# Kernel tuning notes

Hardware: AMD Instinct MI355X
Metric: run time of the kernel (lower is better)

The kernel has to match this reference:

```python
import jax, jax.numpy as jnp
import numpy as np
from jax import lax

INPUT_SIZE = 256
HIDDEN_SIZE = 512
NUM_LAYERS = 2
T = 2048
B = 64


def setup_inputs() -> dict:
    key = jax.random.key(0)
    k1, k2, k3, k4, k5 = jax.random.split(key, 5)
    fan_g = INPUT_SIZE + HIDDEN_SIZE
    inp = {
        "input": jax.random.normal(k1, (T, B, INPUT_SIZE), dtype=jnp.float32),
        "gate_w": jax.random.uniform(k2, (HIDDEN_SIZE, fan_g), dtype=jnp.float32,
                                     minval=-1.0, maxval=1.0) / np.sqrt(fan_g),
        "gate_b": jax.random.uniform(k3, (HIDDEN_SIZE,), dtype=jnp.float32,
                                     minval=-1.0, maxval=1.0) / np.sqrt(fan_g),
        "out_w": jax.random.uniform(k4, (INPUT_SIZE, HIDDEN_SIZE), dtype=jnp.float32,
                                    minval=-1.0, maxval=1.0) / np.sqrt(HIDDEN_SIZE),
        "out_b": jax.random.uniform(k5, (INPUT_SIZE,), dtype=jnp.float32,
                                    minval=-1.0, maxval=1.0) / np.sqrt(HIDDEN_SIZE),
        "name": 0,  # unused forward arg in the original module
    }
    return inp


def reference(input, gate_w, gate_b, out_w, out_b, name):
    # input: [T, B, input_size]
    batch = input.shape[1]
    h0 = jnp.zeros((batch, HIDDEN_SIZE), dtype=jnp.float32)
    c0 = jnp.zeros((batch, HIDDEN_SIZE), dtype=jnp.float32)

    def step(carry, x_t):
        h, c = carry
        combined = jnp.concatenate([h, x_t], axis=1)          # [B, H+I]
        g = combined @ gate_w.T + gate_b
        s = jax.nn.sigmoid(g)                                 # f = i = o = sigmoid(g)
        ch = jnp.tanh(g)                                      # cell_helper
        c = c * s + ch * s
        h = jnp.tanh(c) * s
        return (h, c), None

    carry = (h0, c0)
    # hidden/cell carry over across layers; every layer re-consumes the same input
    for _ in range(NUM_LAYERS):
        carry, _ = lax.scan(step, carry, input)
    h, _ = carry
    output = h @ out_w.T + out_b                              # [B, input_size]
    return output
```

## Files before the change

### kernel.cpp

```cpp
#include <hip/hip_runtime.h>
#include <stdint.h>

#define T_STEPS 2048
#define BATCH   64
#define IN_SZ   256
#define HID     512
#define FANG    768
#define NLAYER  2
#define TOT_STEPS (T_STEPS*NLAYER)

typedef _Float16 h2 __attribute__((ext_vector_type(2)));
typedef unsigned long long u64;
typedef unsigned int u32;

__device__ __forceinline__ float dot2f(h2 a, h2 b, float c) {
#if __has_builtin(__builtin_amdgcn_fdot2)
    return __builtin_amdgcn_fdot2(a, b, c, false);
#else
    return c + (float)a.x * (float)b.x + (float)a.y * (float)b.y;
#endif
}

__device__ __forceinline__ u32 packh2(float a, float b) {
    h2 t{(_Float16)a, (_Float16)b};
    return __builtin_bit_cast(u32, t);
}
__device__ __forceinline__ h2 bch2(float v) { return __builtin_bit_cast(h2, v); }
__device__ __forceinline__ h2 bch2u(u32 v)  { return __builtin_bit_cast(h2, v); }

__device__ __forceinline__ u64 ld_llc(const u64* p) {
    return __hip_atomic_load(p, __ATOMIC_RELAXED, __HIP_MEMORY_SCOPE_AGENT);
}
__device__ __forceinline__ void st_llc(u64* p, u64 v) {
    __hip_atomic_store(p, v, __ATOMIC_RELAXED, __HIP_MEMORY_SCOPE_AGENT);
}

template<int CTRL>
__device__ __forceinline__ float dpp_add(float x) {
    int xi = __builtin_bit_cast(int, x);
    int yi = __builtin_amdgcn_update_dpp(0, xi, CTRL, 0xf, 0xf, true);
    return x + __builtin_bit_cast(float, yi);
}
__device__ __forceinline__ float reduce16(float x) {
    x = dpp_add<0xB1>(x);
    x = dpp_add<0x4E>(x);
    x = dpp_add<0x124>(x);
    x = dpp_add<0x128>(x);
    return x;
}

__global__ __launch_bounds__(256) void xproj_kernel(
    const float* __restrict__ input,
    const float* __restrict__ gate_w,
    const float* __restrict__ gate_b,
    u32* __restrict__ xp16)
{
    __shared__ _Float16 Bs[64][264];
    __shared__ _Float16 As[64][264];

    const int jt = blockIdx.x;
    const int mg = blockIdx.y;
    const int tid = threadIdx.x;
    const int tx = tid & 15, ty = tid >> 4;
    const int j0 = jt * 64;

    #pragma unroll
    for (int l = 0; l < 16; ++l) {
        int e = tid + l * 256;
        int i = e >> 6, kq = e & 63;
        float4 v = *(const float4*)&gate_w[(size_t)(j0 + i) * FANG + HID + kq * 4];
        *(h2*)&Bs[i][kq * 4]     = h2{(_Float16)v.x, (_Float16)v.y};
        *(h2*)&Bs[i][kq * 4 + 2] = h2{(_Float16)v.z, (_Float16)v.w};
    }

    const float4 gb = *(const float4*)&gate_b[j0 + tx * 4];

    for (int mt = 0; mt < 32; ++mt) {
        const int m0 = (mg * 32 + mt) * 64;
        __syncthreads();
        #pragma unroll
        for (int l = 0; l < 16; ++l) {
            int e = tid + l * 256;
            int i = e >> 6, kq = e & 63;
            float4 v = *(const float4*)&input[(size_t)(m0 + i) * IN_SZ + kq * 4];
            *(h2*)&As[i][kq * 4]     = h2{(_Float16)v.x, (_Float16)v.y};
            *(h2*)&As[i][kq * 4 + 2] = h2{(_Float16)v.z, (_Float16)v.w};
        }
        __syncthreads();

        float acc[4][4] = {};
        #pragma unroll
        for (int q = 0; q < 32; ++q) {
            const int k = ((q + tx) & 31) * 8;
            float4 av[4], bv[4];
            #pragma unroll
            for (int i = 0; i < 4; ++i)  av[i] = *(const float4*)&As[ty * 4 + i][k];
            #pragma unroll
            for (int jj = 0; jj < 4; ++jj) bv[jj] = *(const float4*)&Bs[tx * 4 + jj][k];
            #pragma unroll
            for (int i = 0; i < 4; ++i) {
                h2 a0 = bch2(av[i].x), a1 = bch2(av[i].y);
                h2 a2 = bch2(av[i].z), a3 = bch2(av[i].w);
                #pragma unroll
                for (int jj = 0; jj < 4; ++jj) {
                    acc[i][jj] = dot2f(a0, bch2(bv[jj].x), acc[i][jj]);
                    acc[i][jj] = dot2f(a1, bch2(bv[jj].y), acc[i][jj]);
                    acc[i][jj] = dot2f(a2, bch2(bv[jj].z), acc[i][jj]);
                    acc[i][jj] = dot2f(a3, bch2(bv[jj].w), acc[i][jj]);
                }
            }
        }

        #pragma unroll
        for (int i = 0; i < 4; ++i) {
            uint2 ww = { packh2(acc[i][0] + gb.x, acc[i][1] + gb.y),
                         packh2(acc[i][2] + gb.z, acc[i][3] + gb.w) };
            *(uint2*)&xp16[(size_t)(m0 + ty * 4 + i) * 256 + ((j0 + tx * 4) >> 1)] = ww;
        }
    }
}

__global__ __launch_bounds__(512, 2) void lstm_kernel(
    const float* __restrict__ gate_w,
    const u32* __restrict__ xp16,
    u64* __restrict__ hx)
{
    const int blk = blockIdx.x;
    const int s   = blk >> 6;
    const int b   = blk & 63;
    const int tid = threadIdx.x;
    const int g   = tid >> 4;
    const int c   = tid & 15;
    const int j0  = s * 128 + g * 4;

    __shared__ u32 hl[2][256];

    h2 w2[64];
    #pragma unroll
    for (int u = 0; u < 4; ++u) {
        const int kb = (((s + u) & 3) * 64 + c * 4) * 2;
        #pragma unroll
        for (int rr = 0; rr < 4; ++rr) {
            const float* wr = gate_w + (size_t)(j0 + rr) * FANG + kb;
            float4 v0 = *(const float4*)(wr);
            float4 v1 = *(const float4*)(wr + 4);
            w2[rr * 16 + u * 4 + 0] = h2{(_Float16)v0.x, (_Float16)v0.y};
            w2[rr * 16 + u * 4 + 1] = h2{(_Float16)v0.z, (_Float16)v0.w};
            w2[rr * 16 + u * 4 + 2] = h2{(_Float16)v1.x, (_Float16)v1.y};
            w2[rr * 16 + u * 4 + 3] = h2{(_Float16)v1.z, (_Float16)v1.w};
        }
    }

    const int si  = tid >> 6;
    const int qs  = si + (si >= s);
    const int prw = qs * 64 + (tid & 63);

    if (tid < 256) hl[0][tid] = 0;

    float cval = 0.0f;

    for (int st = 0; st < TOT_STEPS; ++st) {
        const int t   = st & (T_STEPS - 1);
        const int buf = st & 1;

        u32 xw = 0;
        if (c < 4) xw = xp16[((size_t)t * BATCH + b) * 256 + s * 64 + g * 2 + (c >> 1)];

        const u64* pp = hx + ((size_t)buf * BATCH + b) * 256 + prw;
        u64 pv = 0;
        if (tid < 192) pv = ld_llc(pp);

        __syncthreads();

        float a0 = 0.f, a1 = 0.f, a2 = 0.f, a3 = 0.f;
        {
            float4 rv = *(const float4*)&hl[buf][s * 64 + c * 4];
            h2 x0 = bch2(rv.x), x1 = bch2(rv.y), x2 = bch2(rv.z), x3 = bch2(rv.w);
            a0 = dot2f(w2[ 0], x0, a0); a0 = dot2f(w2[ 1], x1, a0);
            a0 = dot2f(w2[ 2], x2, a0); a0 = dot2f(w2[ 3], x3, a0);
            a1 = dot2f(w2[16], x0, a1); a1 = dot2f(w2[17], x1, a1);
            a1 = dot2f(w2[18], x2, a1); a1 = dot2f(w2[19], x3, a1);
            a2 = dot2f(w2[32], x0, a2); a2 = dot2f(w2[33], x1, a2);
            a2 = dot2f(w2[34], x2, a2); a2 = dot2f(w2[35], x3, a2);
            a3 = dot2f(w2[48], x0, a3); a3 = dot2f(w2[49], x1, a3);
            a3 = dot2f(w2[50], x2, a3); a3 = dot2f(w2[51], x3, a3);
        }

        if (tid < 192) {
            u64 v = pv;
            int spin = 0;
            while ((u32)(v >> 32) != (u32)st) {
                v = ld_llc(pp);
                if (++spin > (1 << 16)) break;
                if (spin > 64) __builtin_amdgcn_s_sleep(1);
            }
            hl[buf][prw] = (u32)v;
        }
        __syncthreads();

        #pragma unroll
        for (int u = 1; u < 4; ++u) {
            float4 rv = *(const float4*)&hl[buf][((s + u) & 3) * 64 + c * 4];
            h2 x0 = bch2(rv.x), x1 = bch2(rv.y), x2 = bch2(rv.z), x3 = bch2(rv.w);
            a0 = dot2f(w2[     u*4+0], x0, a0); a0 = dot2f(w2[     u*4+1], x1, a0);
            a0 = dot2f(w2[     u*4+2], x2, a0); a0 = dot2f(w2[     u*4+3], x3, a0);
            a1 = dot2f(w2[16 + u*4+0], x0, a1); a1 = dot2f(w2[16 + u*4+1], x1, a1);
            a1 = dot2f(w2[16 + u*4+2], x2, a1); a1 = dot2f(w2[16 + u*4+3], x3, a1);
            a2 = dot2f(w2[32 + u*4+0], x0, a2); a2 = dot2f(w2[32 + u*4+1], x1, a2);
            a2 = dot2f(w2[32 + u*4+2], x2, a2); a2 = dot2f(w2[32 + u*4+3], x3, a2);
            a3 = dot2f(w2[48 + u*4+0], x0, a3); a3 = dot2f(w2[48 + u*4+1], x1, a3);
            a3 = dot2f(w2[48 + u*4+2], x2, a3); a3 = dot2f(w2[48 + u*4+3], x3, a3);
        }

        a0 = reduce16(a0);
        a1 = reduce16(a1);
        a2 = reduce16(a2);
        a3 = reduce16(a3);

        float hf = 0.0f;
        if (c < 4) {
            float p = (c == 0) ? a0 : (c == 1) ? a1 : (c == 2) ? a2 : a3;
            h2 xp = bch2u(xw);
            float gg = p + (float)((c & 1) ? xp.y : xp.x);
            gg = fminf(fmaxf(gg, -30.0f), 30.0f);
            float sg = 1.0f / (1.0f + __expf(-gg));
            float e2 = __expf(2.0f * gg);
            float ch = (e2 - 1.0f) / (e2 + 1.0f);
            cval = cval * sg + ch * sg;
            float ca = fminf(fmaxf(cval, -15.0f), 15.0f);
            float e3 = __expf(2.0f * ca);
            hf = ((e3 - 1.0f) / (e3 + 1.0f)) * sg;
        }
        float hfo = __shfl_down(hf, 1);
        if (c == 0 || c == 2) {
            const int w = s * 64 + g * 2 + (c >> 1);
            u32 pk = packh2(hf, hfo);
            st_llc(hx + ((size_t)((st + 1) & 1) * BATCH + b) * 256 + w,
                   (u64)pk | ((u64)(u32)(st + 1) << 32));
            hl[buf ^ 1][w] = pk;
        }
    }
}

__global__ __launch_bounds__(256) void out_kernel(
    const u64* __restrict__ hx,
    const float* __restrict__ out_w,
    const float* __restrict__ out_b,
    float* __restrict__ out)
{
    const int b  = blockIdx.x;
    const int jt = threadIdx.x;
    __shared__ float hrow[512];

    {
        u64 v = hx[(size_t)b * 256 + jt];
        h2 pr = bch2u((u32)v);
        hrow[2 * jt]     = (float)pr.x;
        hrow[2 * jt + 1] = (float)pr.y;
    }
    __syncthreads();

    float acc = out_b[jt];
    const float* wr = out_w + (size_t)jt * HID;
    #pragma unroll 8
    for (int k = 0; k < HID; ++k)
        acc += hrow[k] * wr[k];
    out[(size_t)b * IN_SZ + jt] = acc;
}

extern "C" void kernel_launch(void* const* d_in, const int* in_sizes, int n_in,
                              void* d_out, int out_size, void* d_ws, size_t ws_size,
                              hipStream_t stream)
{
    const float* input  = (const float*)d_in[0];
    const float* gate_w = (const float*)d_in[1];
    const float* gate_b = (const float*)d_in[2];
    const float* out_w  = (const float*)d_in[3];
    const float* out_b  = (const float*)d_in[4];
    float* out = (float*)d_out;

    u32* xp16 = (u32*)d_ws;
    const size_t xbytes = (size_t)T_STEPS * BATCH * 256 * sizeof(u32);
    u64* hx = (u64*)((char*)d_ws + xbytes);

    (void)hipMemsetAsync(hx, 0, (size_t)2 * BATCH * 256 * sizeof(u64), stream);

    dim3 g1(8, 64);
    xproj_kernel<<<g1, 256, 0, stream>>>(input, gate_w, gate_b, xp16);
    lstm_kernel<<<256, 512, 0, stream>>>(gate_w, xp16, hx);
    out_kernel<<<64, 256, 0, stream>>>(hx, out_w, out_b, out);
}
```

Before: 4.936 ms.

## Drop extra barrier, double-issue spin polls, and use rcp-based activations

```diff
diff --git a/kernel.cpp b/kernel.cpp
--- a/kernel.cpp
+++ b/kernel.cpp
@@ -35,6 +35,12 @@
     __hip_atomic_store(p, v, __ATOMIC_RELAXED, __HIP_MEMORY_SCOPE_AGENT);
 }
 
+__device__ __forceinline__ void wg_barrier() {
+    asm volatile("s_waitcnt lgkmcnt(0)" ::: "memory");
+    __builtin_amdgcn_s_barrier();
+    asm volatile("" ::: "memory");
+}
+
 template<int CTRL>
 __device__ __forceinline__ float dpp_add(float x) {
     int xi = __builtin_bit_cast(int, x);
@@ -47,6 +53,12 @@
     x = dpp_add<0x124>(x);
     x = dpp_add<0x128>(x);
     return x;
+}
+
+__device__ __forceinline__ float rcpf(float x) { return __builtin_amdgcn_rcpf(x); }
+__device__ __forceinline__ float tanh_pos(float ax) {
+    float t = __expf(-2.0f * ax);
+    return (1.0f - t) * rcpf(1.0f + t);
 }
 
 __global__ __launch_bounds__(256) void xproj_kernel(
@@ -166,40 +178,27 @@
         u32 xw = 0;
         if (c < 4) xw = xp16[((size_t)t * BATCH + b) * 256 + s * 64 + g * 2 + (c >> 1)];
 
-        const u64* pp = hx + ((size_t)buf * BATCH + b) * 256 + prw;
-        u64 pv = 0;
-        if (tid < 192) pv = ld_llc(pp);
-
-        __syncthreads();
-
-        float a0 = 0.f, a1 = 0.f, a2 = 0.f, a3 = 0.f;
-        {
-            float4 rv = *(const float4*)&hl[buf][s * 64 + c * 4];
-            h2 x0 = bch2(rv.x), x1 = bch2(rv.y), x2 = bch2(rv.z), x3 = bch2(rv.w);
-            a0 = dot2f(w2[ 0], x0, a0); a0 = dot2f(w2[ 1], x1, a0);
-            a0 = dot2f(w2[ 2], x2, a0); a0 = dot2f(w2[ 3], x3, a0);
-            a1 = dot2f(w2[16], x0, a1); a1 = dot2f(w2[17], x1, a1);
-            a1 = dot2f(w2[18], x2, a1); a1 = dot2f(w2[19], x3, a1);
-            a2 = dot2f(w2[32], x0, a2); a2 = dot2f(w2[33], x1, a2);
-            a2 = dot2f(w2[34], x2, a2); a2 = dot2f(w2[35], x3, a2);
-            a3 = dot2f(w2[48], x0, a3); a3 = dot2f(w2[49], x1, a3);
-            a3 = dot2f(w2[50], x2, a3); a3 = dot2f(w2[51], x3, a3);
-        }
-
         if (tid < 192) {
-            u64 v = pv;
+            const u64* pp = hx + ((size_t)buf * BATCH + b) * 256 + prw;
+            u64 va = ld_llc(pp);
+            u64 vb = ld_llc(pp);
+            u64 v;
             int spin = 0;
-            while ((u32)(v >> 32) != (u32)st) {
-                v = ld_llc(pp);
-                if (++spin > (1 << 16)) break;
-                if (spin > 64) __builtin_amdgcn_s_sleep(1);
+            for (;;) {
+                if ((u32)(va >> 32) == (u32)st) { v = va; break; }
+                va = ld_llc(pp);
+                if ((u32)(vb >> 32) == (u32)st) { v = vb; break; }
+                vb = ld_llc(pp);
+                if (++spin > (1 << 15)) { v = va; break; }
             }
             hl[buf][prw] = (u32)v;
         }
-        __syncthreads();
-
-        #pragma unroll
-        for (int u = 1; u < 4; ++u) {
+
+        wg_barrier();
+
+        float a0 = 0.f, a1 = 0.f, a2 = 0.f, a3 = 0.f;
+        #pragma unroll
+        for (int u = 0; u < 4; ++u) {
             float4 rv = *(const float4*)&hl[buf][((s + u) & 3) * 64 + c * 4];
             h2 x0 = bch2(rv.x), x1 = bch2(rv.y), x2 = bch2(rv.z), x3 = bch2(rv.w);
             a0 = dot2f(w2[     u*4+0], x0, a0); a0 = dot2f(w2[     u*4+1], x1, a0);
@@ -222,14 +221,12 @@
             float p = (c == 0) ? a0 : (c == 1) ? a1 : (c == 2) ? a2 : a3;
             h2 xp = bch2u(xw);
             float gg = p + (float)((c & 1) ? xp.y : xp.x);
-            gg = fminf(fmaxf(gg, -30.0f), 30.0f);
-            float sg = 1.0f / (1.0f + __expf(-gg));
-            float e2 = __expf(2.0f * gg);
-            float ch = (e2 - 1.0f) / (e2 + 1.0f);
-            cval = cval * sg + ch * sg;
-            float ca = fminf(fmaxf(cval, -15.0f), 15.0f);
-            float e3 = __expf(2.0f * ca);
-            hf = ((e3 - 1.0f) / (e3 + 1.0f)) * sg;
+            float et = __expf(-gg);
+            float sg = rcpf(1.0f + et);
+            float ch = copysignf(tanh_pos(fabsf(gg)), gg);
+            cval = (cval + ch) * sg;
+            float th = copysignf(tanh_pos(fabsf(cval)), cval);
+            hf = th * sg;
         }
         float hfo = __shfl_down(hf, 1);
         if (c == 0 || c == 2) {
```

Result: slower. 5.617 ms (+13.8%).

## Spread polling across all waves, lighter barriers, cheaper activation math

Applied to the files above, without the earlier changes.

```diff
diff --git a/kernel.cpp b/kernel.cpp
--- a/kernel.cpp
+++ b/kernel.cpp
@@ -35,6 +35,12 @@
     __hip_atomic_store(p, v, __ATOMIC_RELAXED, __HIP_MEMORY_SCOPE_AGENT);
 }
 
+__device__ __forceinline__ void wg_barrier() {
+    asm volatile("s_waitcnt lgkmcnt(0)" ::: "memory");
+    __builtin_amdgcn_s_barrier();
+    asm volatile("" ::: "memory");
+}
+
 template<int CTRL>
 __device__ __forceinline__ float dpp_add(float x) {
     int xi = __builtin_bit_cast(int, x);
@@ -47,6 +53,12 @@
     x = dpp_add<0x124>(x);
     x = dpp_add<0x128>(x);
     return x;
+}
+
+__device__ __forceinline__ float rcpf(float x) { return __builtin_amdgcn_rcpf(x); }
+__device__ __forceinline__ float tanh_pos(float ax) {
+    float t = __expf(-2.0f * ax);
+    return (1.0f - t) * rcpf(1.0f + t);
 }
 
 __global__ __launch_bounds__(256) void xproj_kernel(
@@ -125,13 +137,15 @@
     const u32* __restrict__ xp16,
     u64* __restrict__ hx)
 {
-    const int blk = blockIdx.x;
-    const int s   = blk >> 6;
-    const int b   = blk & 63;
-    const int tid = threadIdx.x;
-    const int g   = tid >> 4;
-    const int c   = tid & 15;
-    const int j0  = s * 128 + g * 4;
+    const int blk  = blockIdx.x;
+    const int s    = blk >> 6;
+    const int b    = blk & 63;
+    const int tid  = threadIdx.x;
+    const int g    = tid >> 4;
+    const int c    = tid & 15;
+    const int wv   = tid >> 6;
+    const int lane = tid & 63;
+    const int j0   = s * 128 + g * 4;
 
     __shared__ u32 hl[2][256];
 
@@ -151,9 +165,11 @@
         }
     }
 
-    const int si  = tid >> 6;
-    const int qs  = si + (si >= s);
-    const int prw = qs * 64 + (tid & 63);
+    const bool poller = (lane < 24);
+    const int  pi  = wv * 24 + lane;
+    const int  si  = pi >> 6;
+    const int  qs  = si + (si >= s);
+    const int  prw = qs * 64 + (pi & 63);
 
     if (tid < 256) hl[0][tid] = 0;
 
@@ -168,9 +184,9 @@
 
         const u64* pp = hx + ((size_t)buf * BATCH + b) * 256 + prw;
         u64 pv = 0;
-        if (tid < 192) pv = ld_llc(pp);
-
-        __syncthreads();
+        if (poller) pv = ld_llc(pp);
+
+        wg_barrier();
 
         float a0 = 0.f, a1 = 0.f, a2 = 0.f, a3 = 0.f;
         {
@@ -186,7 +202,7 @@
             a3 = dot2f(w2[50], x2, a3); a3 = dot2f(w2[51], x3, a3);
         }
 
-        if (tid < 192) {
+        if (poller) {
             u64 v = pv;
             int spin = 0;
             while ((u32)(v >> 32) != (u32)st) {
@@ -196,7 +212,7 @@
             }
             hl[buf][prw] = (u32)v;
         }
-        __syncthreads();
+        wg_barrier();
 
         #pragma unroll
         for (int u = 1; u < 4; ++u) {
@@ -222,14 +238,12 @@
             float p = (c == 0) ? a0 : (c == 1) ? a1 : (c == 2) ? a2 : a3;
             h2 xp = bch2u(xw);
             float gg = p + (float)((c & 1) ? xp.y : xp.x);
-            gg = fminf(fmaxf(gg, -30.0f), 30.0f);
-            float sg = 1.0f / (1.0f + __expf(-gg));
-            float e2 = __expf(2.0f * gg);
-            float ch = (e2 - 1.0f) / (e2 + 1.0f);
-            cval = cval * sg + ch * sg;
-            float ca = fminf(fmaxf(cval, -15.0f), 15.0f);
-            float e3 = __expf(2.0f * ca);
-            hf = ((e3 - 1.0f) / (e3 + 1.0f)) * sg;
+            float et = __expf(-gg);
+            float sg = rcpf(1.0f + et);
+            float ch = copysignf(tanh_pos(fabsf(gg)), gg);
+            cval = (cval + ch) * sg;
+            float th = copysignf(tanh_pos(fabsf(cval)), cval);
+            hf = th * sg;
         }
         float hfo = __shfl_down(hf, 1);
         if (c == 0 || c == 2) {
```

Measured after the change: 5.064 ms. 1.03x slower.
